# Optimization experiments

Measured on AMD Instinct MI355X. Metric: run time of the kernel, lower is better.

## Reference

```python
import jax, jax.numpy as jnp
import numpy as np

B, T, D = 32, 1024, 1024
N, L = 77, 768
H = 8
TED = 2048  # time_embed_dim
EPS = 1e-5


def _ln(x, g, b):
    m = jnp.mean(x, axis=-1, keepdims=True)
    v = jnp.var(x, axis=-1, keepdims=True)
    return (x - m) * jax.lax.rsqrt(v + EPS) * g + b


def setup_inputs() -> dict:
    key = jax.random.key(0)
    ks = jax.random.split(key, 16)
    s = lambda fan_in: 1.0 / np.sqrt(fan_in)
    return {
        "x": jax.random.normal(ks[0], (B, T, D), jnp.float32),
        "xf": jax.random.normal(ks[1], (B, N, L), jnp.float32),
        "emb": jax.random.normal(ks[2], (B, TED), jnp.float32),
        "norm_g": jnp.ones((D,), jnp.float32),
        "norm_b": jnp.zeros((D,), jnp.float32),
        "tnorm_g": jnp.ones((L,), jnp.float32),
        "tnorm_b": jnp.zeros((L,), jnp.float32),
        "Wq": jax.random.normal(ks[3], (D, D), jnp.float32) * s(D),
        "bq": jnp.zeros((D,), jnp.float32),
        "Wk": jax.random.normal(ks[4], (L, D), jnp.float32) * s(L),
        "bk": jnp.zeros((D,), jnp.float32),
        "Wv": jax.random.normal(ks[5], (L, D), jnp.float32) * s(L),
        "bv": jnp.zeros((D,), jnp.float32),
        "emb_W": jax.random.normal(ks[6], (TED, 2 * D), jnp.float32) * s(TED),
        "emb_b": jnp.zeros((2 * D,), jnp.float32),
        "onorm_g": jnp.ones((D,), jnp.float32),
        "onorm_b": jnp.zeros((D,), jnp.float32),
        "Wo": jax.random.normal(ks[7], (D, D), jnp.float32) * s(D),
        "bo": jnp.zeros((D,), jnp.float32),
    }


def reference(x, xf, emb, norm_g, norm_b, tnorm_g, tnorm_b, Wq, bq, Wk, bk, Wv, bv,
              emb_W, emb_b, onorm_g, onorm_b, Wo, bo):
    Bc, Tc, Dc = x.shape
    Nc = xf.shape[1]
    hd = Dc // H
    # projections
    q = _ln(x, norm_g, norm_b) @ Wq + bq                      # [B,T,D]
    xfn = _ln(xf, tnorm_g, tnorm_b)                           # [B,N,L]
    k = (xfn @ Wk + bk).reshape(Bc, Nc, H, hd)                # [B,N,H,hd]
    v = (xfn @ Wv + bv).reshape(Bc, Nc, H, hd)                # [B,N,H,hd]
    q = jax.nn.softmax(q.reshape(Bc, Tc, H, hd), axis=-1)     # softmax over head_dim
    k = jax.nn.softmax(k, axis=1)                             # softmax over N (key tokens)
    # linear-attention: no TxN matrix
    attn = jnp.einsum('bnhd,bnhl->bhdl', k, v)                # [B,H,hd,hd]
    y = jnp.einsum('bthd,bhdl->bthl', q, attn).reshape(Bc, Tc, Dc)
    # StylizationBlock
    emb_out = jax.nn.silu(emb) @ emb_W + emb_b                # [B,2D]
    scale, shift = jnp.split(emb_out[:, None, :], 2, axis=2)  # [B,1,D] each
    h = _ln(y, onorm_g, onorm_b) * (1.0 + scale) + shift
    h = jax.nn.silu(h) @ Wo + bo
    return x + h
```

## Files before the change

kernel.cpp:

```cpp
#include <hip/hip_runtime.h>
#include <hip/hip_bf16.h>
#include <math.h>

namespace {

constexpr int Bc  = 32;
constexpr int Tc  = 1024;
constexpr int Dc  = 1024;
constexpr int Nt  = 77;
constexpr int Lc  = 768;
constexpr int HDc = 128;
constexpr int TEDc = 2048;
constexpr float EPSc = 1e-5f;

typedef __attribute__((ext_vector_type(8))) short bf16x8;
typedef __attribute__((ext_vector_type(8))) unsigned short u16x8;
typedef __attribute__((ext_vector_type(4))) float f32x4;

__device__ __forceinline__ float silu_f(float x) { return x / (1.f + __expf(-x)); }

__device__ __forceinline__ unsigned short f2bf(float f) {
  unsigned u = __float_as_uint(f);
  return (unsigned short)((u + 0x7fffu + ((u >> 16) & 1u)) >> 16);
}
__device__ __forceinline__ float bf2f(unsigned short h) {
  return __uint_as_float(((unsigned)h) << 16);
}

__device__ __forceinline__ void gload16(const void* g, void* l) {
  __builtin_amdgcn_global_load_lds((const __attribute__((address_space(1))) void*)g,
                                   (__attribute__((address_space(3))) void*)l, 16, 0, 0);
}

__device__ __forceinline__ int rowswz(int r) {
  return (((r >> 3) & 1) << 1) | ((r >> 1) & 1);
}

__global__ __launch_bounds__(256) void ln_bf16_kernel(
    const float* __restrict__ src, unsigned short* __restrict__ dst, int cols,
    const float* __restrict__ g, const float* __restrict__ b)
{
  const int row = blockIdx.x;
  const float* p = src + (size_t)row * cols;
  const int c = threadIdx.x * 4;
  float4 v = make_float4(0.f, 0.f, 0.f, 0.f);
  if (c < cols) v = *reinterpret_cast<const float4*>(p + c);
  float s  = v.x + v.y + v.z + v.w;
  float sq = v.x * v.x + v.y * v.y + v.z * v.z + v.w * v.w;
  __shared__ float red[2][4];
  __shared__ float mr[2];
  for (int o = 32; o > 0; o >>= 1) { s += __shfl_down(s, o); sq += __shfl_down(sq, o); }
  const int wid = threadIdx.x >> 6, lane = threadIdx.x & 63;
  if (lane == 0) { red[0][wid] = s; red[1][wid] = sq; }
  __syncthreads();
  if (threadIdx.x == 0) {
    const float S  = red[0][0] + red[0][1] + red[0][2] + red[0][3];
    const float SQ = red[1][0] + red[1][1] + red[1][2] + red[1][3];
    const float mean = S / cols;
    const float var  = SQ / cols - mean * mean;
    mr[0] = mean; mr[1] = rsqrtf(var + EPSc);
  }
  __syncthreads();
  if (c < cols) {
    const float mean = mr[0], rstd = mr[1];
    ushort4 o;
    o.x = f2bf((v.x - mean) * rstd * g[c + 0] + b[c + 0]);
    o.y = f2bf((v.y - mean) * rstd * g[c + 1] + b[c + 1]);
    o.z = f2bf((v.z - mean) * rstd * g[c + 2] + b[c + 2]);
    o.w = f2bf((v.w - mean) * rstd * g[c + 3] + b[c + 3]);
    *reinterpret_cast<ushort4*>(dst + (size_t)row * cols + c) = o;
  }
}

__global__ __launch_bounds__(256) void convT_bf16_kernel(
    const float* __restrict__ W, unsigned short* __restrict__ Wt, int K, int N)
{
  __shared__ float t[32][33];
  const int n0 = blockIdx.x * 32, k0 = blockIdx.y * 32;
  const int tx = threadIdx.x & 31, ty = threadIdx.x >> 5;
  #pragma unroll
  for (int dy = 0; dy < 32; dy += 8)
    t[ty + dy][tx] = W[(size_t)(k0 + ty + dy) * N + n0 + tx];
  __syncthreads();
  #pragma unroll
  for (int dy = 0; dy < 32; dy += 8)
    Wt[(size_t)(n0 + ty + dy) * K + k0 + tx] = f2bf(t[tx][ty + dy]);
}

__global__ __launch_bounds__(256) void convT2_bf16_kernel(
    const float* __restrict__ W0, unsigned short* __restrict__ T0,
    const float* __restrict__ W1, unsigned short* __restrict__ T1, int K, int N)
{
  __shared__ float t[32][33];
  const float* W = blockIdx.z ? W1 : W0;
  unsigned short* Wt = blockIdx.z ? T1 : T0;
  const int n0 = blockIdx.x * 32, k0 = blockIdx.y * 32;
  const int tx = threadIdx.x & 31, ty = threadIdx.x >> 5;
  #pragma unroll
  for (int dy = 0; dy < 32; dy += 8)
    t[ty + dy][tx] = W[(size_t)(k0 + ty + dy) * N + n0 + tx];
  __syncthreads();
  #pragma unroll
  for (int dy = 0; dy < 32; dy += 8)
    Wt[(size_t)(n0 + ty + dy) * K + k0 + tx] = f2bf(t[tx][ty + dy]);
}

template<int EPI>
__global__ __launch_bounds__(512, 2) void gemm2_kernel(
    const unsigned short* __restrict__ A, const unsigned short* __restrict__ Bt,
    const float* __restrict__ bias, const float* __restrict__ bias2, int bsplit,
    void* __restrict__ Cout, int M, int K, int N, const float* __restrict__ xres)
{
  __shared__ unsigned short lds[32768];
  const int tid = threadIdx.x, wid = tid >> 6, lane = tid & 63;
  const int ntx = N >> 8;
  int swz = blockIdx.x;
  const int nwg = gridDim.x;
  if ((nwg & 7) == 0) { const int cpx = nwg >> 3; swz = (swz & 7) * cpx + (swz >> 3); }
  const int bx = swz % ntx, by = swz / ntx;
  const int bm0 = by << 8, bn0 = bx << 8;
  const int wr = wid >> 2, wc = wid & 3, lhi = lane >> 4, llo = lane & 15;

  const int srow = lane >> 2;
  const int scol = (((lane & 3) ^ rowswz(srow)) * 8);
  int ar0 = bm0 + wid * 32 + srow;      if (ar0 >= M) ar0 = M - 1;
  int ar1 = bm0 + wid * 32 + 16 + srow; if (ar1 >= M) ar1 = M - 1;
  const int br0 = bn0 + wid * 32 + srow;
  const int br1 = br0 + 16;
  const unsigned short* Ag0 = A  + (size_t)ar0 * K + scol;
  const unsigned short* Ag1 = A  + (size_t)ar1 * K + scol;
  const unsigned short* Bg0 = Bt + (size_t)br0 * K + scol;
  const unsigned short* Bg1 = Bt + (size_t)br1 * K + scol;
  const int lc0 = (wid * 2) * 512, lc1 = (wid * 2 + 1) * 512;
  const int rx = rowswz(llo);
  const int aoff = wr * 8 * 512 + llo * 32 + ((lhi ^ rx) * 8);
  const int boff = wc * 4 * 512 + llo * 32 + ((lhi ^ rx) * 8);

  f32x4 acc[8][4] = {};
  const int nt = K >> 5;

  gload16(Ag0, &lds[lc0]);
  gload16(Ag1, &lds[lc1]);
  gload16(Bg0, &lds[16384 + lc0]);
  gload16(Bg1, &lds[16384 + lc1]);
  __syncthreads();

  int cur = 0;
  for (int t = 1; t < nt; ++t) {
    const int nb = cur ^ 1;
    const int k0 = t << 5;
    gload16(Ag0 + k0, &lds[nb * 8192 + lc0]);
    gload16(Ag1 + k0, &lds[nb * 8192 + lc1]);
    gload16(Bg0 + k0, &lds[16384 + nb * 8192 + lc0]);
    gload16(Bg1 + k0, &lds[16384 + nb * 8192 + lc1]);
    bf16x8 a_[8], b_[4];
    #pragma unroll
    for (int mi = 0; mi < 8; mi++) a_[mi] = *(const bf16x8*)(&lds[cur * 8192 + aoff + mi * 512]);
    #pragma unroll
    for (int ni = 0; ni < 4; ni++) b_[ni] = *(const bf16x8*)(&lds[16384 + cur * 8192 + boff + ni * 512]);
    #pragma unroll
    for (int mi = 0; mi < 8; mi++)
      #pragma unroll
      for (int ni = 0; ni < 4; ni++)
        acc[mi][ni] = __builtin_amdgcn_mfma_f32_16x16x32_bf16(a_[mi], b_[ni], acc[mi][ni], 0, 0, 0);
    __syncthreads();
    cur = nb;
  }
  {
    bf16x8 a_[8], b_[4];
    #pragma unroll
    for (int mi = 0; mi < 8; mi++) a_[mi] = *(const bf16x8*)(&lds[cur * 8192 + aoff + mi * 512]);
    #pragma unroll
    for (int ni = 0; ni < 4; ni++) b_[ni] = *(const bf16x8*)(&lds[16384 + cur * 8192 + boff + ni * 512]);
    #pragma unroll
    for (int mi = 0; mi < 8; mi++)
      #pragma unroll
      for (int ni = 0; ni < 4; ni++)
        acc[mi][ni] = __builtin_amdgcn_mfma_f32_16x16x32_bf16(a_[mi], b_[ni], acc[mi][ni], 0, 0, 0);
  }

  if constexpr (EPI != 2) {
    #pragma unroll
    for (int mi = 0; mi < 8; mi++) {
      #pragma unroll
      for (int ni = 0; ni < 4; ni++) {
        const int col = bn0 + wc * 64 + ni * 16 + llo;
        const float bs = (bsplit > 0 && col >= bsplit) ? bias2[col - bsplit] : bias[col];
        #pragma unroll
        for (int r = 0; r < 4; r++) {
          const int row = bm0 + wr * 128 + mi * 16 + lhi * 4 + r;
          if (row < M) {
            float v = acc[mi][ni][r] + bs;
            if (EPI == 1) v += xres[(size_t)row * N + col];
            ((float*)Cout)[(size_t)row * N + col] = v;
          }
        }
      }
    }
  } else {
    unsigned short* Cb = (unsigned short*)Cout;
    __syncthreads();
    #pragma unroll
    for (int h = 0; h < 2; ++h) {
      if ((wc >> 1) == h) {
        #pragma unroll
        for (int mi = 0; mi < 8; mi++) {
          #pragma unroll
          for (int ni = 0; ni < 4; ni++) {
            const int lcol = (wc & 1) * 64 + ni * 16 + llo;
            const float bs = bias[bn0 + h * 128 + lcol];
            #pragma unroll
            for (int r = 0; r < 4; r++) {
              const int lrow = wr * 128 + mi * 16 + lhi * 4 + r;
              lds[lrow * 128 + (lcol ^ ((lrow & 7) << 3))] = f2bf(acc[mi][ni][r] + bs);
            }
          }
        }
      }
      __syncthreads();
      const int row = tid >> 1, cb = (tid & 1) * 64;
      const int sw = (row & 7) << 3;
      float mx = -1e30f;
      #pragma unroll
      for (int g = 0; g < 8; g++) {
        u16x8 u = *(const u16x8*)(&lds[row * 128 + ((cb + g * 8) ^ sw)]);
        #pragma unroll
        for (int j = 0; j < 8; j++) mx = fmaxf(mx, bf2f(u[j]));
      }
      mx = fmaxf(mx, __shfl_xor(mx, 1));
      float ssum = 0.f;
      float ev[8][8];
      #pragma unroll
      for (int g = 0; g < 8; g++) {
        u16x8 u = *(const u16x8*)(&lds[row * 128 + ((cb + g * 8) ^ sw)]);
        #pragma unroll
        for (int j = 0; j < 8; j++) { ev[g][j] = __expf(bf2f(u[j]) - mx); ssum += ev[g][j]; }
      }
      ssum += __shfl_xor(ssum, 1);
      const float inv = 1.f / ssum;
      #pragma unroll
      for (int g = 0; g < 8; g++) {
        u16x8 o;
        #pragma unroll
        for (int j = 0; j < 8; j++) o[j] = f2bf(ev[g][j] * inv);
        *(u16x8*)(&Cb[(size_t)(bm0 + row) * N + bn0 + h * 128 + cb + g * 8]) = o;
      }
      __syncthreads();
    }
  }
}

__global__ void softmax_k_kernel(float* __restrict__ kv) {
  const int idx = blockIdx.x * blockDim.x + threadIdx.x;
  const int b = idx >> 10, d = idx & 1023;
  float* p = kv + (size_t)b * Nt * 2048 + d;
  float m = -1e30f;
  for (int n = 0; n < Nt; n++) m = fmaxf(m, p[(size_t)n * 2048]);
  float s = 0.f;
  for (int n = 0; n < Nt; n++) s += __expf(p[(size_t)n * 2048] - m);
  const float inv = 1.f / s;
  for (int n = 0; n < Nt; n++) p[(size_t)n * 2048] = __expf(p[(size_t)n * 2048] - m) * inv;
}

__global__ __launch_bounds__(256) void attn_einsum_kernel(
    const float* __restrict__ kv, unsigned short* __restrict__ attnT) {
  const int bh = blockIdx.x;
  const int b = bh >> 3, h = bh & 7;
  __shared__ float ks[Nt][HDc];
  __shared__ float vs[Nt][HDc];
  const float* kb = kv + (size_t)b * Nt * 2048 + h * HDc;
  const float* vb = kv + (size_t)b * Nt * 2048 + 1024 + h * HDc;
  for (int i = threadIdx.x; i < Nt * HDc; i += 256) {
    const int n = i >> 7, d = i & 127;
    ks[n][d] = kb[(size_t)n * 2048 + d];
    vs[n][d] = vb[(size_t)n * 2048 + d];
  }
  __syncthreads();
  const int tx = threadIdx.x & 15, ty = threadIdx.x >> 4;
  float acc[8][8] = {};
  for (int n = 0; n < Nt; n++) {
    float a[8], w[8];
    #pragma unroll
    for (int i = 0; i < 8; i++) a[i] = vs[n][ty + 16 * i];
    #pragma unroll
    for (int j = 0; j < 8; j++) w[j] = ks[n][tx + 16 * j];
    #pragma unroll
    for (int i = 0; i < 8; i++)
      #pragma unroll
      for (int j = 0; j < 8; j++)
        acc[i][j] += a[i] * w[j];
  }
  unsigned short* ab = attnT + (size_t)bh * HDc * HDc;
  #pragma unroll
  for (int i = 0; i < 8; i++)
    #pragma unroll
    for (int j = 0; j < 8; j++)
      ab[(size_t)(ty + 16 * i) * HDc + tx + 16 * j] = f2bf(acc[i][j]);
}

__global__ __launch_bounds__(256) void y_mfma_kernel(
    unsigned short* __restrict__ q, const unsigned short* __restrict__ attnT)
{
  __shared__ unsigned short lds[16384];
  const int tid = threadIdx.x, wid = tid >> 6, lane = tid & 63;
  const int bh = blockIdx.y, b = bh >> 3, h = bh & 7;
  const int bm0 = blockIdx.x << 7;
  const int wr = wid >> 1, wc = wid & 1, lhi = lane >> 4, llo = lane & 15;

  unsigned short* Abase = q + ((size_t)b * Tc) * Dc + h * HDc;
  const unsigned short* Btb = attnT + (size_t)bh * HDc * HDc;

  const int srow = lane >> 2;
  const int scol = (((lane & 3) ^ rowswz(srow)) * 8);
  const int ar0 = bm0 + wid * 32 + srow, ar1 = ar0 + 16;
  const int br0 = wid * 32 + srow,       br1 = br0 + 16;
  const unsigned short* Ag0 = Abase + (size_t)ar0 * Dc + scol;
  const unsigned short* Ag1 = Abase + (size_t)ar1 * Dc + scol;
  const unsigned short* Bg0 = Btb + (size_t)br0 * HDc + scol;
  const unsigned short* Bg1 = Btb + (size_t)br1 * HDc + scol;
  const int lc0 = (wid * 2 + 0) * 512, lc1 = (wid * 2 + 1) * 512;
  const int rx = rowswz(llo);
  const int aoff = wr * 2048 + llo * 32 + ((lhi ^ rx) * 8);
  const int boff = wc * 2048 + llo * 32 + ((lhi ^ rx) * 8);

  f32x4 acc[4][4] = {};

  gload16(Ag0, &lds[lc0]);
  gload16(Ag1, &lds[lc1]);
  gload16(Bg0, &lds[8192 + lc0]);
  gload16(Bg1, &lds[8192 + lc1]);
  __syncthreads();

  int cur = 0;
  for (int t = 1; t < 4; ++t) {
    const int nb = cur ^ 1;
    const int k0 = t << 5;
    gload16(Ag0 + k0, &lds[nb * 4096 + lc0]);
    gload16(Ag1 + k0, &lds[nb * 4096 + lc1]);
    gload16(Bg0 + k0, &lds[8192 + nb * 4096 + lc0]);
    gload16(Bg1 + k0, &lds[8192 + nb * 4096 + lc1]);
    bf16x8 a_[4], b_[4];
    #pragma unroll
    for (int mi = 0; mi < 4; mi++) a_[mi] = *(const bf16x8*)(&lds[cur * 4096 + aoff + mi * 512]);
    #pragma unroll
    for (int ni = 0; ni < 4; ni++) b_[ni] = *(const bf16x8*)(&lds[8192 + cur * 4096 + boff + ni * 512]);
    #pragma unroll
    for (int mi = 0; mi < 4; mi++)
      #pragma unroll
      for (int ni = 0; ni < 4; ni++)
        acc[mi][ni] = __builtin_amdgcn_mfma_f32_16x16x32_bf16(a_[mi], b_[ni], acc[mi][ni], 0, 0, 0);
    __syncthreads();
    cur = nb;
  }
  {
    bf16x8 a_[4], b_[4];
    #pragma unroll
    for (int mi = 0; mi < 4; mi++) a_[mi] = *(const bf16x8*)(&lds[cur * 4096 + aoff + mi * 512]);
    #pragma unroll
    for (int ni = 0; ni < 4; ni++) b_[ni] = *(const bf16x8*)(&lds[8192 + cur * 4096 + boff + ni * 512]);
    #pragma unroll
    for (int mi = 0; mi < 4; mi++)
      #pragma unroll
      for (int ni = 0; ni < 4; ni++)
        acc[mi][ni] = __builtin_amdgcn_mfma_f32_16x16x32_bf16(a_[mi], b_[ni], acc[mi][ni], 0, 0, 0);
  }

  __syncthreads();
  #pragma unroll
  for (int mi = 0; mi < 4; mi++) {
    #pragma unroll
    for (int ni = 0; ni < 4; ni++) {
      const int col = wc * 64 + ni * 16 + llo;
      #pragma unroll
      for (int r = 0; r < 4; r++) {
        const int row = wr * 64 + mi * 16 + lhi * 4 + r;
        lds[row * 128 + (col ^ ((row & 7) << 3))] = f2bf(acc[mi][ni][r]);
      }
    }
  }
  __syncthreads();
  const int row = tid >> 1, cb = (tid & 1) * 64;
  const int sw = (row & 7) << 3;
  #pragma unroll
  for (int g = 0; g < 8; g++) {
    u16x8 u = *(const u16x8*)(&lds[row * 128 + ((cb + g * 8) ^ sw)]);
    *(u16x8*)(&Abase[(size_t)(bm0 + row) * Dc + cb + g * 8]) = u;
  }
}

__global__ __launch_bounds__(256) void ln_mod_silu_bf16_kernel(
    unsigned short* __restrict__ y, const float* __restrict__ ss,
    const float* __restrict__ g, const float* __restrict__ bvec) {
  const int row = blockIdx.x;
  const int b = row >> 10;
  unsigned short* p = y + (size_t)row * Dc;
  const int c = threadIdx.x * 4;
  ushort4 u = *reinterpret_cast<const ushort4*>(p + c);
  float vv[4] = {bf2f(u.x), bf2f(u.y), bf2f(u.z), bf2f(u.w)};
  float s  = vv[0] + vv[1] + vv[2] + vv[3];
  float sq = vv[0]*vv[0] + vv[1]*vv[1] + vv[2]*vv[2] + vv[3]*vv[3];
  __shared__ float red[2][4];
  __shared__ float mr[2];
  for (int o = 32; o > 0; o >>= 1) { s += __shfl_down(s, o); sq += __shfl_down(sq, o); }
  const int wid = threadIdx.x >> 6, lane = threadIdx.x & 63;
  if (lane == 0) { red[0][wid] = s; red[1][wid] = sq; }
  __syncthreads();
  if (threadIdx.x == 0) {
    const float S  = red[0][0] + red[0][1] + red[0][2] + red[0][3];
    const float SQ = red[1][0] + red[1][1] + red[1][2] + red[1][3];
    const float mean = S / Dc;
    const float var = SQ / Dc - mean * mean;
    mr[0] = mean; mr[1] = rsqrtf(var + EPSc);
  }
  __syncthreads();
  const float mean = mr[0], rstd = mr[1];
  const float* ssb = ss + (size_t)b * 2 * Dc;
  ushort4 o;
  float t0 = (vv[0] - mean) * rstd * g[c + 0] + bvec[c + 0];
  float t1 = (vv[1] - mean) * rstd * g[c + 1] + bvec[c + 1];
  float t2 = (vv[2] - mean) * rstd * g[c + 2] + bvec[c + 2];
  float t3 = (vv[3] - mean) * rstd * g[c + 3] + bvec[c + 3];
  o.x = f2bf(silu_f(t0 * (1.f + ssb[c + 0]) + ssb[Dc + c + 0]));
  o.y = f2bf(silu_f(t1 * (1.f + ssb[c + 1]) + ssb[Dc + c + 1]));
  o.z = f2bf(silu_f(t2 * (1.f + ssb[c + 2]) + ssb[Dc + c + 2]));
  o.w = f2bf(silu_f(t3 * (1.f + ssb[c + 3]) + ssb[Dc + c + 3]));
  *reinterpret_cast<ushort4*>(p + c) = o;
}

__global__ __launch_bounds__(256) void silu_emb_kernel(
    const float* __restrict__ emb, float* __restrict__ sile) {
  const int i = (blockIdx.x * 256 + threadIdx.x) * 4;
  float4 v = *reinterpret_cast<const float4*>(emb + i);
  v.x = silu_f(v.x); v.y = silu_f(v.y); v.z = silu_f(v.z); v.w = silu_f(v.w);
  *reinterpret_cast<float4*>(sile + i) = v;
}

__global__ __launch_bounds__(256) void emb_part_kernel(
    const float* __restrict__ sile, const float* __restrict__ W,
    float* __restrict__ part) {
  const int split = blockIdx.y;
  const int n = blockIdx.x * 256 + threadIdx.x;
  const int k0 = split * 64;
  const float* se = sile + k0;
  const float* Wp = W + (size_t)k0 * (2 * Dc) + n;
  float acc[32] = {};
  for (int kk = 0; kk < 64; kk++) {
    const float w = Wp[(size_t)kk * (2 * Dc)];
    #pragma unroll
    for (int m = 0; m < 32; m++)
      acc[m] = fmaf(se[m * TEDc + kk], w, acc[m]);
  }
  float* pp = part + (size_t)split * 32 * (2 * Dc) + n;
  #pragma unroll
  for (int m = 0; m < 32; m++) pp[(size_t)m * (2 * Dc)] = acc[m];
}

__global__ __launch_bounds__(256) void emb_reduce_kernel(
    const float* __restrict__ part, const float* __restrict__ bias,
    float* __restrict__ ssb) {
  const int i = blockIdx.x * 256 + threadIdx.x;
  const int n = i & (2 * Dc - 1);
  float s = bias[n];
  #pragma unroll 8
  for (int sp = 0; sp < 32; sp++) s += part[(size_t)sp * 32 * (2 * Dc) + i];
  ssb[i] = s;
}

}

extern "C" void kernel_launch(void* const* d_in, const int* in_sizes, int n_in,
                              void* d_out, int out_size, void* d_ws, size_t ws_size,
                              hipStream_t stream) {
  const float* x       = (const float*)d_in[0];
  const float* xf      = (const float*)d_in[1];
  const float* emb     = (const float*)d_in[2];
  const float* norm_g  = (const float*)d_in[3];
  const float* norm_b  = (const float*)d_in[4];
  const float* tnorm_g = (const float*)d_in[5];
  const float* tnorm_b = (const float*)d_in[6];
  const float* Wq      = (const float*)d_in[7];
  const float* bq      = (const float*)d_in[8];
  const float* Wk      = (const float*)d_in[9];
  const float* bk      = (const float*)d_in[10];
  const float* Wv      = (const float*)d_in[11];
  const float* bv_     = (const float*)d_in[12];
  const float* emb_W   = (const float*)d_in[13];
  const float* emb_b   = (const float*)d_in[14];
  const float* onorm_g = (const float*)d_in[15];
  const float* onorm_b = (const float*)d_in[16];
  const float* Wo      = (const float*)d_in[17];
  const float* bo      = (const float*)d_in[18];
  float* out = (float*)d_out;

  char* ws = (char*)d_ws;
  unsigned short* Ab = (unsigned short*)ws;
  char* R = ws;
  unsigned short* qb   = (unsigned short*)(ws + 67108864);
  unsigned short* Wq_t = (unsigned short*)(ws + 134217728);
  unsigned short* Wk_t = (unsigned short*)(ws + 136314880);
  unsigned short* Wv_t = (unsigned short*)(ws + 137887744);
  unsigned short* Wo_t = (unsigned short*)(ws + 139460608);
  float*          ssb  = (float*)(ws + 141557760);
  float*          sile = (float*)(ws + 141819904);
  float*          part = (float*)(ws + 142082048);
  unsigned short* xfb   = (unsigned short*)(R);
  float*          kv    = (float*)(R + 3784704);
  unsigned short* attnT = (unsigned short*)(R + 23969792);

  const int Mq  = Bc * Tc;
  const int Mkv = Bc * Nt;

  ln_bf16_kernel<<<Mq, 256, 0, stream>>>(x, Ab, Dc, norm_g, norm_b);
  convT_bf16_kernel<<<dim3(Dc / 32, Dc / 32), 256, 0, stream>>>(Wq, Wq_t, Dc, Dc);
  convT2_bf16_kernel<<<dim3(Dc / 32, Lc / 32, 2), 256, 0, stream>>>(Wk, Wk_t, Wv, Wv_t, Lc, Dc);
  convT_bf16_kernel<<<dim3(Dc / 32, Dc / 32), 256, 0, stream>>>(Wo, Wo_t, Dc, Dc);

  gemm2_kernel<2><<<(Dc / 256) * (Mq / 256), 512, 0, stream>>>(
      Ab, Wq_t, bq, nullptr, 0, qb, Mq, Dc, Dc, nullptr);

  ln_bf16_kernel<<<Mkv, 256, 0, stream>>>(xf, xfb, Lc, tnorm_g, tnorm_b);
  gemm2_kernel<0><<<(2048 / 256) * ((Mkv + 255) / 256), 512, 0, stream>>>(
      xfb, Wk_t, bk, bv_, 1024, kv, Mkv, Lc, 2048, nullptr);
  softmax_k_kernel<<<(Bc * Dc) / 256, 256, 0, stream>>>(kv);
  attn_einsum_kernel<<<Bc * 8, 256, 0, stream>>>(kv, attnT);

  silu_emb_kernel<<<(Bc * TEDc) / 1024, 256, 0, stream>>>(emb, sile);
  emb_part_kernel<<<dim3(8, 32), 256, 0, stream>>>(sile, emb_W, part);
  emb_reduce_kernel<<<(Bc * 2 * Dc) / 256, 256, 0, stream>>>(part, emb_b, ssb);

  y_mfma_kernel<<<dim3(Tc / 128, Bc * 8), 256, 0, stream>>>(qb, attnT);
  ln_mod_silu_bf16_kernel<<<Mq, 256, 0, stream>>>(qb, ssb, onorm_g, onorm_b);
  gemm2_kernel<1><<<(Dc / 256) * (Mq / 256), 512, 0, stream>>>(
      qb, Wo_t, bo, nullptr, 0, out, Mq, Dc, Dc, x);
}
```

Measured before the change: 524.5 us.

## Double GEMM K-tile to 64 with new LDS swizzle; fuse key softmax into attention

The main GEMM now stages 64-wide K tiles (128 KB LDS, double-buffered) with an 8-way XOR swizzle, halving the number of barriers per K. It also raises wave priority around the MFMA block and drops a redundant barrier in the softmax epilogue. The separate key-softmax kernel is folded into the attention einsum kernel, where the softmax runs on data already held in shared memory, removing one global pass over k. The y kernel loses its LDS swizzle, which may reintroduce bank conflicts. The larger LDS footprint may reduce the number of workgroups resident per CU despite launch_bounds(512,2).

```diff
diff --git a/kernel.cpp b/kernel.cpp
--- a/kernel.cpp
+++ b/kernel.cpp
@@ -30,10 +30,6 @@
 __device__ __forceinline__ void gload16(const void* g, void* l) {
   __builtin_amdgcn_global_load_lds((const __attribute__((address_space(1))) void*)g,
                                    (__attribute__((address_space(3))) void*)l, 16, 0, 0);
-}
-
-__device__ __forceinline__ int rowswz(int r) {
-  return (((r >> 3) & 1) << 1) | ((r >> 1) & 1);
 }
 
 __global__ __launch_bounds__(256) void ln_bf16_kernel(
@@ -106,12 +102,12 @@
 }
 
 template<int EPI>
-__global__ __launch_bounds__(512, 2) void gemm2_kernel(
+__global__ __launch_bounds__(512, 2) void gemm3_kernel(
     const unsigned short* __restrict__ A, const unsigned short* __restrict__ Bt,
     const float* __restrict__ bias, const float* __restrict__ bias2, int bsplit,
     void* __restrict__ Cout, int M, int K, int N, const float* __restrict__ xres)
 {
-  __shared__ unsigned short lds[32768];
+  __shared__ unsigned short lds[65536];
   const int tid = threadIdx.x, wid = tid >> 6, lane = tid & 63;
   const int ntx = N >> 8;
   int swz = blockIdx.x;
@@ -121,62 +117,75 @@
   const int bm0 = by << 8, bn0 = bx << 8;
   const int wr = wid >> 2, wc = wid & 3, lhi = lane >> 4, llo = lane & 15;
 
-  const int srow = lane >> 2;
-  const int scol = (((lane & 3) ^ rowswz(srow)) * 8);
-  int ar0 = bm0 + wid * 32 + srow;      if (ar0 >= M) ar0 = M - 1;
-  int ar1 = bm0 + wid * 32 + 16 + srow; if (ar1 >= M) ar1 = M - 1;
-  const int br0 = bn0 + wid * 32 + srow;
-  const int br1 = br0 + 16;
-  const unsigned short* Ag0 = A  + (size_t)ar0 * K + scol;
-  const unsigned short* Ag1 = A  + (size_t)ar1 * K + scol;
-  const unsigned short* Bg0 = Bt + (size_t)br0 * K + scol;
-  const unsigned short* Bg1 = Bt + (size_t)br1 * K + scol;
-  const int lc0 = (wid * 2) * 512, lc1 = (wid * 2 + 1) * 512;
-  const int rx = rowswz(llo);
-  const int aoff = wr * 8 * 512 + llo * 32 + ((lhi ^ rx) * 8);
-  const int boff = wc * 4 * 512 + llo * 32 + ((lhi ^ rx) * 8);
+  const int srow = wid * 8 + (lane >> 3);
+  const int spc  = (((lane & 7) ^ ((lane >> 3) & 7))) * 8;
+  const unsigned short* Agp[4];
+  const unsigned short* Bgp[4];
+  #pragma unroll
+  for (int j = 0; j < 4; j++) {
+    int ra = bm0 + j * 64 + srow; if (ra >= M) ra = M - 1;
+    Agp[j] = A  + (size_t)ra * K + spc;
+    Bgp[j] = Bt + (size_t)(bn0 + j * 64 + srow) * K + spc;
+  }
+  const int sll = llo & 7;
+  const int abase = (wr * 128 + llo) * 64;
+  const int bbase = (wc * 64 + llo) * 64;
+  const int pk0 = ((0 + lhi) ^ sll) * 8;
+  const int pk1 = ((4 + lhi) ^ sll) * 8;
 
   f32x4 acc[8][4] = {};
-  const int nt = K >> 5;
-
-  gload16(Ag0, &lds[lc0]);
-  gload16(Ag1, &lds[lc1]);
-  gload16(Bg0, &lds[16384 + lc0]);
-  gload16(Bg1, &lds[16384 + lc1]);
+  const int nt = K >> 6;
+
+  #pragma unroll
+  for (int j = 0; j < 4; j++) {
+    gload16(Agp[j], &lds[j * 4096 + wid * 512]);
+    gload16(Bgp[j], &lds[32768 + j * 4096 + wid * 512]);
+  }
   __syncthreads();
 
   int cur = 0;
-  for (int t = 1; t < nt; ++t) {
+  for (int t = 0; t < nt; ++t) {
     const int nb = cur ^ 1;
-    const int k0 = t << 5;
-    gload16(Ag0 + k0, &lds[nb * 8192 + lc0]);
-    gload16(Ag1 + k0, &lds[nb * 8192 + lc1]);
-    gload16(Bg0 + k0, &lds[16384 + nb * 8192 + lc0]);
-    gload16(Bg1 + k0, &lds[16384 + nb * 8192 + lc1]);
-    bf16x8 a_[8], b_[4];
-    #pragma unroll
-    for (int mi = 0; mi < 8; mi++) a_[mi] = *(const bf16x8*)(&lds[cur * 8192 + aoff + mi * 512]);
-    #pragma unroll
-    for (int ni = 0; ni < 4; ni++) b_[ni] = *(const bf16x8*)(&lds[16384 + cur * 8192 + boff + ni * 512]);
-    #pragma unroll
-    for (int mi = 0; mi < 8; mi++)
+    if (t + 1 < nt) {
+      const int k0 = (t + 1) << 6;
+      #pragma unroll
+      for (int j = 0; j < 4; j++) {
+        gload16(Agp[j] + k0, &lds[nb * 16384 + j * 4096 + wid * 512]);
+        gload16(Bgp[j] + k0, &lds[32768 + nb * 16384 + j * 4096 + wid * 512]);
+      }
+    }
+    __builtin_amdgcn_s_setprio(1);
+    {
+      bf16x8 a_[8], b_[4];
+      #pragma unroll
+      for (int mi = 0; mi < 8; mi++)
+        a_[mi] = *(const bf16x8*)(&lds[cur * 16384 + abase + mi * 1024 + pk0]);
       #pragma unroll
       for (int ni = 0; ni < 4; ni++)
-        acc[mi][ni] = __builtin_amdgcn_mfma_f32_16x16x32_bf16(a_[mi], b_[ni], acc[mi][ni], 0, 0, 0);
+        b_[ni] = *(const bf16x8*)(&lds[32768 + cur * 16384 + bbase + ni * 1024 + pk0]);
+      #pragma unroll
+      for (int mi = 0; mi < 8; mi++)
+        #pragma unroll
+        for (int ni = 0; ni < 4; ni++)
+          acc[mi][ni] = __builtin_amdgcn_mfma_f32_16x16x32_bf16(a_[mi], b_[ni], acc[mi][ni], 0, 0, 0);
+    }
+    {
+      bf16x8 a_[8], b_[4];
+      #pragma unroll
+      for (int mi = 0; mi < 8; mi++)
+        a_[mi] = *(const bf16x8*)(&lds[cur * 16384 + abase + mi * 1024 + pk1]);
+      #pragma unroll
+      for (int ni = 0; ni < 4; ni++)
+        b_[ni] = *(const bf16x8*)(&lds[32768 + cur * 16384 + bbase + ni * 1024 + pk1]);
+      #pragma unroll
+      for (int mi = 0; mi < 8; mi++)
+        #pragma unroll
+        for (int ni = 0; ni < 4; ni++)
+          acc[mi][ni] = __builtin_amdgcn_mfma_f32_16x16x32_bf16(a_[mi], b_[ni], acc[mi][ni], 0, 0, 0);
+    }
+    __builtin_amdgcn_s_setprio(0);
     __syncthreads();
     cur = nb;
-  }
-  {
-    bf16x8 a_[8], b_[4];
-    #pragma unroll
-    for (int mi = 0; mi < 8; mi++) a_[mi] = *(const bf16x8*)(&lds[cur * 8192 + aoff + mi * 512]);
-    #pragma unroll
-    for (int ni = 0; ni < 4; ni++) b_[ni] = *(const bf16x8*)(&lds[16384 + cur * 8192 + boff + ni * 512]);
-    #pragma unroll
-    for (int mi = 0; mi < 8; mi++)
-      #pragma unroll
-      for (int ni = 0; ni < 4; ni++)
-        acc[mi][ni] = __builtin_amdgcn_mfma_f32_16x16x32_bf16(a_[mi], b_[ni], acc[mi][ni], 0, 0, 0);
   }
 
   if constexpr (EPI != 2) {
@@ -199,7 +208,6 @@
     }
   } else {
     unsigned short* Cb = (unsigned short*)Cout;
-    __syncthreads();
     #pragma unroll
     for (int h = 0; h < 2; ++h) {
       if ((wc >> 1) == h) {
@@ -218,12 +226,12 @@
         }
       }
       __syncthreads();
-      const int row = tid >> 1, cb = (tid & 1) * 64;
+      const int row = tid >> 1, cb2 = (tid & 1) * 64;
       const int sw = (row & 7) << 3;
       float mx = -1e30f;
       #pragma unroll
       for (int g = 0; g < 8; g++) {
-        u16x8 u = *(const u16x8*)(&lds[row * 128 + ((cb + g * 8) ^ sw)]);
+        u16x8 u = *(const u16x8*)(&lds[row * 128 + ((cb2 + g * 8) ^ sw)]);
         #pragma unroll
         for (int j = 0; j < 8; j++) mx = fmaxf(mx, bf2f(u[j]));
       }
@@ -232,7 +240,7 @@
       float ev[8][8];
       #pragma unroll
       for (int g = 0; g < 8; g++) {
-        u16x8 u = *(const u16x8*)(&lds[row * 128 + ((cb + g * 8) ^ sw)]);
+        u16x8 u = *(const u16x8*)(&lds[row * 128 + ((cb2 + g * 8) ^ sw)]);
         #pragma unroll
         for (int j = 0; j < 8; j++) { ev[g][j] = __expf(bf2f(u[j]) - mx); ssum += ev[g][j]; }
       }
@@ -243,26 +251,14 @@
         u16x8 o;
         #pragma unroll
         for (int j = 0; j < 8; j++) o[j] = f2bf(ev[g][j] * inv);
-        *(u16x8*)(&Cb[(size_t)(bm0 + row) * N + bn0 + h * 128 + cb + g * 8]) = o;
+        *(u16x8*)(&Cb[(size_t)(bm0 + row) * N + bn0 + h * 128 + cb2 + g * 8]) = o;
       }
       __syncthreads();
     }
   }
 }
 
-__global__ void softmax_k_kernel(float* __restrict__ kv) {
-  const int idx = blockIdx.x * blockDim.x + threadIdx.x;
-  const int b = idx >> 10, d = idx & 1023;
-  float* p = kv + (size_t)b * Nt * 2048 + d;
-  float m = -1e30f;
-  for (int n = 0; n < Nt; n++) m = fmaxf(m, p[(size_t)n * 2048]);
-  float s = 0.f;
-  for (int n = 0; n < Nt; n++) s += __expf(p[(size_t)n * 2048] - m);
-  const float inv = 1.f / s;
-  for (int n = 0; n < Nt; n++) p[(size_t)n * 2048] = __expf(p[(size_t)n * 2048] - m) * inv;
-}
-
-__global__ __launch_bounds__(256) void attn_einsum_kernel(
+__global__ __launch_bounds__(256) void attn_fused_kernel(
     const float* __restrict__ kv, unsigned short* __restrict__ attnT) {
   const int bh = blockIdx.x;
   const int b = bh >> 3, h = bh & 7;
@@ -276,6 +272,16 @@
     vs[n][d] = vb[(size_t)n * 2048 + d];
   }
   __syncthreads();
+  if (threadIdx.x < HDc) {
+    const int d = threadIdx.x;
+    float m = -1e30f;
+    for (int n = 0; n < Nt; n++) m = fmaxf(m, ks[n][d]);
+    float s = 0.f;
+    for (int n = 0; n < Nt; n++) { float e = __expf(ks[n][d] - m); ks[n][d] = e; s += e; }
+    const float inv = 1.f / s;
+    for (int n = 0; n < Nt; n++) ks[n][d] *= inv;
+  }
+  __syncthreads();
   const int tx = threadIdx.x & 15, ty = threadIdx.x >> 4;
   float acc[8][8] = {};
   for (int n = 0; n < Nt; n++) {
@@ -310,8 +316,7 @@
   unsigned short* Abase = q + ((size_t)b * Tc) * Dc + h * HDc;
   const unsigned short* Btb = attnT + (size_t)bh * HDc * HDc;
 
-  const int srow = lane >> 2;
-  const int scol = (((lane & 3) ^ rowswz(srow)) * 8);
+  const int srow = lane >> 2, scol = (lane & 3) * 8;
   const int ar0 = bm0 + wid * 32 + srow, ar1 = ar0 + 16;
   const int br0 = wid * 32 + srow,       br1 = br0 + 16;
   const unsigned short* Ag0 = Abase + (size_t)ar0 * Dc + scol;
@@ -319,9 +324,8 @@
   const unsigned short* Bg0 = Btb + (size_t)br0 * HDc + scol;
   const unsigned short* Bg1 = Btb + (size_t)br1 * HDc + scol;
   const int lc0 = (wid * 2 + 0) * 512, lc1 = (wid * 2 + 1) * 512;
-  const int rx = rowswz(llo);
-  const int aoff = wr * 2048 + llo * 32 + ((lhi ^ rx) * 8);
-  const int boff = wc * 2048 + llo * 32 + ((lhi ^ rx) * 8);
+  const int aoff = wr * 2048 + llo * 32 + lhi * 8;
+  const int boff = wc * 2048 + llo * 32 + lhi * 8;
 
   f32x4 acc[4][4] = {};
 
@@ -515,14 +519,13 @@
   convT2_bf16_kernel<<<dim3(Dc / 32, Lc / 32, 2), 256, 0, stream>>>(Wk, Wk_t, Wv, Wv_t, Lc, Dc);
   convT_bf16_kernel<<<dim3(Dc / 32, Dc / 32), 256, 0, stream>>>(Wo, Wo_t, Dc, Dc);
 
-  gemm2_kernel<2><<<(Dc / 256) * (Mq / 256), 512, 0, stream>>>(
+  gemm3_kernel<2><<<(Dc / 256) * (Mq / 256), 512, 0, stream>>>(
       Ab, Wq_t, bq, nullptr, 0, qb, Mq, Dc, Dc, nullptr);
 
   ln_bf16_kernel<<<Mkv, 256, 0, stream>>>(xf, xfb, Lc, tnorm_g, tnorm_b);
-  gemm2_kernel<0><<<(2048 / 256) * ((Mkv + 255) / 256), 512, 0, stream>>>(
+  gemm3_kernel<0><<<(2048 / 256) * ((Mkv + 255) / 256), 512, 0, stream>>>(
       xfb, Wk_t, bk, bv_, 1024, kv, Mkv, Lc, 2048, nullptr);
-  softmax_k_kernel<<<(Bc * Dc) / 256, 256, 0, stream>>>(kv);
-  attn_einsum_kernel<<<Bc * 8, 256, 0, stream>>>(kv, attnT);
+  attn_fused_kernel<<<Bc * 8, 256, 0, stream>>>(kv, attnT);
 
   silu_emb_kernel<<<(Bc * TEDc) / 1024, 256, 0, stream>>>(emb, sile);
   emb_part_kernel<<<dim3(8, 32), 256, 0, stream>>>(sile, emb_W, part);
@@ -530,6 +533,6 @@
 
   y_mfma_kernel<<<dim3(Tc / 128, Bc * 8), 256, 0, stream>>>(qb, attnT);
   ln_mod_silu_bf16_kernel<<<Mq, 256, 0, stream>>>(qb, ssb, onorm_g, onorm_b);
-  gemm2_kernel<1><<<(Dc / 256) * (Mq / 256), 512, 0, stream>>>(
+  gemm3_kernel<1><<<(Dc / 256) * (Mq / 256), 512, 0, stream>>>(
       qb, Wo_t, bo, nullptr, 0, out, Mq, Dc, Dc, x);
 }
```

New measurement: 510.5 us. 1.03x faster.
